# Performance work log

Hardware: AMD Instinct MI355X
Metric: run time of the kernel (lower is better)

## Reference

```python
import jax, jax.numpy as jnp
import numpy as np

N_NODES = 10000
N_EDGES = 80000
D = 512
L = 5
ALPHA = 0.1  # LeakyReLU slope inside GraphAttention
ACT_ALPHA = 0.1  # outer activation slope
EPS = 1e-5
W_SCALE = 0.05  # ~ xavier_normal gain 1.414 for fan_in+fan_out=1536


def leaky(x, a):
    return jnp.where(x >= 0, x, a * x)


def setup_inputs() -> dict:
    key = jax.random.key(0)
    ks = jax.random.split(key, 9)
    return {
        "node_feats": jax.random.normal(ks[0], (N_NODES, D), jnp.float32),
        "edge_feats": jax.random.normal(ks[1], (N_EDGES, D), jnp.float32),
        "src": jax.random.randint(ks[2], (N_EDGES,), 0, N_NODES, jnp.int32),
        "dst": jax.random.randint(ks[3], (N_EDGES,), 0, N_NODES, jnp.int32),
        "Wa": jax.random.normal(ks[4], (L, 2 * D, D), jnp.float32) * W_SCALE,
        "Wn": jax.random.normal(ks[5], (L, 2 * D, D), jnp.float32) * W_SCALE,
        "We": jax.random.normal(ks[6], (L, 2 * D, D), jnp.float32) * W_SCALE,
        "Wnc": jax.random.normal(ks[7], (D, 55), jnp.float32) * W_SCALE,
        "Wec": jax.random.normal(ks[8], (D, 2), jnp.float32) * W_SCALE,
    }


def reference(node_feats, edge_feats, src, dst, Wa, Wn, We, Wnc, Wec):
    n = node_feats.shape[0]
    nx, ex = node_feats, edge_feats
    for l in range(L):
        nx_src = nx[src]  # [E, D]
        nx_dst = nx[dst]  # [E, D]
        # a_p = exp(fa([e_x, dst_x]) - columnwise max over edges)
        ap = jnp.concatenate((ex, nx_dst), axis=1) @ Wa[l]
        ap = jnp.exp(ap - jnp.max(ap, axis=0, keepdims=True))
        # a_r = exp(fa([e_x, src_x]) - columnwise max over edges)
        ar = jnp.concatenate((ex, nx_src), axis=1) @ Wa[l]
        ar = jnp.exp(ar - jnp.max(ar, axis=0, keepdims=True))
        # softmax-like normalization per destination node
        z = jax.ops.segment_sum(ap, dst, num_segments=n)  # [N, D]
        a = ap / (z[dst] + EPS)
        # aggregate a * edge_x to destination nodes
        z2 = jax.ops.segment_sum(a * ex, dst, num_segments=n)  # [N, D]
        ft = jnp.concatenate((z2, nx), axis=1) @ Wn[l]
        # edge update: blend src/dst node feats by a_r/a_p shares
        a_sum = ap + ar
        blend = (ar / a_sum) * nx_src + (ap / a_sum) * nx_dst
        ex_new = jnp.concatenate((blend, ex), axis=1) @ We[l]
        # inner leaky_relu then outer activation (both LeakyReLU)
        nx = leaky(leaky(ft, ALPHA), ACT_ALPHA)
        ex = leaky(leaky(ex_new, ALPHA), ACT_ALPHA)
    node_conf = nx @ Wnc
    edge_conf = ex @ Wec
    return (nx, node_conf, ex, edge_conf)
```

## Files before the change

kernel.cpp:

```cpp
#include <hip/hip_runtime.h>
#include <hip/hip_fp16.h>
#include <math.h>

#define D 512
#define NNODES 10000
#define NEDGES 80000
#define LAYERS 5
#define EPS 1e-5f
#define PPAN 625

typedef _Float16 f16x8 __attribute__((ext_vector_type(8)));
typedef float f32x4 __attribute__((ext_vector_type(4)));

__device__ inline unsigned short f2h(float x) { return __half_as_ushort(__float2half(x)); }
__device__ inline float h2f(unsigned short u) { return __half2float(__ushort_as_half(u)); }
__device__ inline uint4 pack8(const unsigned short* v) {
  uint4 r;
  r.x = (unsigned)v[0] | ((unsigned)v[1] << 16);
  r.y = (unsigned)v[2] | ((unsigned)v[3] << 16);
  r.z = (unsigned)v[4] | ((unsigned)v[5] << 16);
  r.w = (unsigned)v[6] | ((unsigned)v[7] << 16);
  return r;
}
__device__ inline void unpack8(uint4 v, unsigned short* o) {
  o[0] = v.x & 0xffff; o[1] = v.x >> 16;
  o[2] = v.y & 0xffff; o[3] = v.y >> 16;
  o[4] = v.z & 0xffff; o[5] = v.z >> 16;
  o[6] = v.w & 0xffff; o[7] = v.w >> 16;
}

__device__ inline void gload16(const void* g, void* l) {
  __builtin_amdgcn_global_load_lds((const __attribute__((address_space(1))) void*)g,
                                   (__attribute__((address_space(3))) void*)l, 16, 0, 0);
}

__device__ inline int octA(int r, int o) {
  return ((o >> 2) << 6) + ((((o & 3) ^ ((r >> 1) & 3))) << 4);
}

__global__ __launch_bounds__(256) void toF16_k(const float* __restrict__ src,
                                               char* __restrict__ dst, int nOct) {
  for (long long i = (long long)blockIdx.x * 256 + threadIdx.x; i < nOct;
       i += (long long)gridDim.x * 256) {
    int row = (int)(i >> 6), oct = (int)(i & 63);
    const float* s = src + (size_t)row * 512 + oct * 8;
    float4 x0 = *(const float4*)s, x1 = *(const float4*)(s + 4);
    float xs[8] = {x0.x, x0.y, x0.z, x0.w, x1.x, x1.y, x1.z, x1.w};
    unsigned short h[8];
#pragma unroll
    for (int j = 0; j < 8; j++) h[j] = f2h(xs[j]);
    *(uint4*)(dst + (size_t)row * 1024 + octA(row, oct)) = pack8(h);
  }
}

__global__ __launch_bounds__(256) void wprep_k(const float* __restrict__ Wa,
                                               const float* __restrict__ Wn,
                                               const float* __restrict__ We,
                                               char* __restrict__ WT) {
  __shared__ float tile[64][65];
  int mat = blockIdx.z;
  const float* W = (mat < 5) ? Wa + (size_t)mat * 1024 * 512
                 : (mat < 10) ? Wn + (size_t)(mat - 5) * 1024 * 512
                              : We + (size_t)(mat - 10) * 1024 * 512;
  char* out = WT + (size_t)mat * 512 * 2048;
  int n0 = blockIdx.x * 64, k0 = blockIdx.y * 64;
  int t = threadIdx.x;
  int ty = t >> 2, tx = t & 3;
  const float* wr = W + (size_t)(k0 + ty) * 512 + n0 + tx * 16;
  float4 v0 = *(const float4*)(wr + 0), v1 = *(const float4*)(wr + 4);
  float4 v2 = *(const float4*)(wr + 8), v3 = *(const float4*)(wr + 12);
  float vv[16] = {v0.x, v0.y, v0.z, v0.w, v1.x, v1.y, v1.z, v1.w,
                  v2.x, v2.y, v2.z, v2.w, v3.x, v3.y, v3.z, v3.w};
#pragma unroll
  for (int j = 0; j < 16; j++) tile[ty][tx * 16 + j] = vv[j];
  __syncthreads();
#pragma unroll
  for (int p = 0; p < 2; p++) {
    int chunk = t + p * 256;
    int n = chunk >> 3, cc = chunk & 7;
    float xs[8];
#pragma unroll
    for (int j = 0; j < 8; j++) xs[j] = tile[cc * 8 + j][n];
    unsigned short h[8];
#pragma unroll
    for (int j = 0; j < 8; j++) h[j] = f2h(xs[j]);
    int ng = n0 + n;
    int kc = (k0 >> 3) + cc;
    *(uint4*)(out + (size_t)ng * 2048 + octA(ng, kc)) = pack8(h);
  }
}

__global__ __launch_bounds__(256) void hist_k(const int* __restrict__ dst, int* __restrict__ cnt) {
  int e = blockIdx.x * 256 + threadIdx.x;
  if (e < NEDGES) atomicAdd(&cnt[dst[e]], 1);
}

__global__ __launch_bounds__(256) void scan_k(const int* __restrict__ cnt,
                                              int* __restrict__ off, int* __restrict__ cur) {
  __shared__ int part[256];
  const int CH = (NNODES + 255) / 256;
  int t = threadIdx.x;
  int s = 0;
  int l0 = t * CH;
  for (int i = 0; i < CH; i++) {
    int idx = l0 + i;
    if (idx < NNODES) s += cnt[idx];
  }
  part[t] = s;
  __syncthreads();
  if (t == 0) {
    int acc = 0;
    for (int i = 0; i < 256; i++) { int v = part[i]; part[i] = acc; acc += v; }
  }
  __syncthreads();
  int acc = part[t];
  for (int i = 0; i < CH; i++) {
    int idx = l0 + i;
    if (idx < NNODES) { off[idx] = acc; cur[idx] = acc; acc += cnt[idx]; }
  }
  if (t == 255) off[NNODES] = acc;
}

__global__ __launch_bounds__(256) void scatter_k(const int* __restrict__ dst,
                                                 int* __restrict__ cur, int* __restrict__ eid) {
  int e = blockIdx.x * 256 + threadIdx.x;
  if (e < NEDGES) {
    int p = atomicAdd(&cur[dst[e]], 1);
    eid[p] = e;
  }
}

template<int KT, bool ACT, bool OUT_I, bool CMAX, int BM>
__global__ __launch_bounds__(BM * 2) void gemmI(const char* __restrict__ X1,
                                                const char* __restrict__ X2,
                                                const char* __restrict__ BW, int cb0,
                                                void* __restrict__ Yout, int R,
                                                const int* __restrict__ srcI,
                                                const int* __restrict__ dstI,
                                                const char* __restrict__ NaH,
                                                float* __restrict__ part_p,
                                                float* __restrict__ part_r) {
  constexpr int T = BM * 2;
  constexpr int BUF = (BM == 256) ? 24576 : 16384;
  constexpr int BOFF = (BM == 256) ? 16384 : 8192;
  constexpr int NH = BM / 64;
  constexpr int G = T / 32;
  __shared__ char smem[3 * BUF];
  const int tid = threadIdx.x;
  const int lane = tid & 63, wv = tid >> 6;
  const int NT = KT / 32;
  int flat = blockIdx.y * 4 + blockIdx.x;
  int total = gridDim.y * 4;
  int xcd = flat & 7, idx = flat >> 3;
  int q = total >> 3, rem = total & 7;
  int base = xcd * q + (xcd < rem ? xcd : rem);
  int f2 = base + idx;
  const int bn0 = (f2 & 3) * 128, bm0 = (f2 >> 2) * BM;
  const int r16 = lane & 15, g = lane >> 4;
  const int mo = (wv >> 1) * 64, no = (wv & 1) * 64;
  const int lr16 = lane >> 2, ls16 = (lane & 3) * 16;
  f32x4 acc[4][4];
#pragma unroll
  for (int i = 0; i < 4; i++)
#pragma unroll
    for (int j = 0; j < 4; j++) acc[i][j] = (f32x4){0.f, 0.f, 0.f, 0.f};

  int offA[4], offB[4];
#pragma unroll
  for (int mi = 0; mi < 4; mi++) {
    int row = mo + mi * 16 + r16;
    offA[mi] = row * 64 + ((g ^ ((row >> 1) & 3)) << 4);
  }
#pragma unroll
  for (int ni = 0; ni < 4; ni++) {
    int row = no + ni * 16 + r16;
    offB[ni] = BOFF + row * 64 + ((g ^ ((row >> 1) & 3)) << 4);
  }

  const char* pA0;
  const char* pA1;
  const char* pB0;
  const char* pB1;
  {
    int g0 = bm0 + wv * 16 + lr16; if (g0 > R - 1) g0 = R - 1;
    int g1 = bm0 + (BM / 2) + wv * 16 + lr16; if (g1 > R - 1) g1 = R - 1;
    pA0 = X1 + (size_t)g0 * 1024 + ls16;
    pA1 = X1 + (size_t)g1 * 1024 + ls16;
    int n0r = bn0 + wv * 16 + lr16;
    pB0 = BW + (size_t)n0r * 2048 + cb0 * 16 + ls16;
    if (BM == 128) {
      int n1r = bn0 + (4 + wv) * 16 + lr16;
      pB1 = BW + (size_t)n1r * 2048 + cb0 * 16 + ls16;
    } else {
      pB1 = pB0;
    }
  }

  int us = 0;
#define STAGE()                                                 \
  {                                                             \
    char* sb = smem + (us % 3) * BUF;                           \
    gload16(pA0, sb + wv * 1024);                               \
    gload16(pA1, sb + ((BM / 32) + wv) * 1024);                 \
    gload16(pB0, sb + BOFF + wv * 1024);                        \
    if (BM == 128) gload16(pB1, sb + BOFF + (4 + wv) * 1024);   \
    pA0 += 64; pA1 += 64; pB0 += 64;                            \
    if (BM == 128) pB1 += 64;                                   \
    us++;                                                       \
  }

  STAGE();
  STAGE();
  for (int t = 0; t < NT; ++t) {
    if (t + 1 < NT) {
      if (BM == 128) asm volatile("s_waitcnt vmcnt(4)" ::: "memory");
      else           asm volatile("s_waitcnt vmcnt(3)" ::: "memory");
    } else {
      asm volatile("s_waitcnt vmcnt(0)" ::: "memory");
    }
    __builtin_amdgcn_s_barrier();
    if (us < NT) {
      if (KT == 1024 && us == 16) {
        int g0 = bm0 + wv * 16 + lr16; if (g0 > R - 1) g0 = R - 1;
        int g1 = bm0 + (BM / 2) + wv * 16 + lr16; if (g1 > R - 1) g1 = R - 1;
        pA0 = X2 + (size_t)g0 * 1024 + ls16;
        pA1 = X2 + (size_t)g1 * 1024 + ls16;
      }
      STAGE();
    }
    const char* As = smem + (t % 3) * BUF;
    f16x8 a[4], b[4];
#pragma unroll
    for (int mi = 0; mi < 4; mi++) a[mi] = *(const f16x8*)(As + offA[mi]);
#pragma unroll
    for (int ni = 0; ni < 4; ni++) b[ni] = *(const f16x8*)(As + offB[ni]);
    __builtin_amdgcn_s_setprio(1);
#pragma unroll
    for (int mi = 0; mi < 4; mi++)
#pragma unroll
      for (int ni = 0; ni < 4; ni++)
        acc[mi][ni] = __builtin_amdgcn_mfma_f32_16x16x32_f16(a[mi], b[ni], acc[mi][ni], 0, 0, 0);
    __builtin_amdgcn_s_setprio(0);
  }
#undef STAGE

  if (!OUT_I) {
    float* Y = (float*)Yout;
#pragma unroll
    for (int mi = 0; mi < 4; mi++)
#pragma unroll
      for (int j = 0; j < 4; j++) {
        int row = bm0 + mo + mi * 16 + g * 4 + j;
        if (row < R) {
#pragma unroll
          for (int ni = 0; ni < 4; ni++) {
            float v = acc[mi][ni][j];
            if (ACT) v = (v >= 0.f) ? v : 0.01f * v;
            Y[(size_t)row * 512 + bn0 + no + ni * 16 + r16] = v;
          }
        }
      }
  } else {
    float* stg = (float*)smem;
    const int hc = tid & 31;
    const int rg = tid >> 5;
    const int coct = (bn0 >> 3) + (hc >> 1);
    const int csub = (hc & 1) * 8;
    float4 mp4 = make_float4(-1e30f, -1e30f, -1e30f, -1e30f);
    float4 mr4 = mp4;
#pragma unroll
    for (int h = 0; h < NH; h++) {
      __syncthreads();
      if ((wv >> 1) == h) {
#pragma unroll
        for (int mi = 0; mi < 4; mi++)
#pragma unroll
          for (int j = 0; j < 4; j++) {
            int rl = mi * 16 + g * 4 + j;
#pragma unroll
            for (int ni = 0; ni < 4; ni++) {
              float v = acc[mi][ni][j];
              if (ACT) v = (v >= 0.f) ? v : 0.01f * v;
              stg[rl * 128 + no + ni * 16 + r16] = v;
            }
          }
      }
      __syncthreads();
#pragma unroll
      for (int qq = 0; qq < 2048 / T; qq++) {
        int rl = rg + qq * G;
        int grow = bm0 + h * 64 + rl;
        if (grow < R) {
          float4 v = *(const float4*)&stg[rl * 128 + hc * 4];
          unsigned short h0 = f2h(v.x), h1 = f2h(v.y), h2 = f2h(v.z), h3 = f2h(v.w);
          uint2 pk;
          pk.x = (unsigned)h0 | ((unsigned)h1 << 16);
          pk.y = (unsigned)h2 | ((unsigned)h3 << 16);
          int oct = (bn0 >> 3) + (hc >> 1);
          *(uint2*)((char*)Yout + (size_t)grow * 1024 + octA(grow, oct) + (hc & 1) * 8) = pk;
          if (CMAX) {
            int d = dstI[grow], s = srcI[grow];
            float qx = h2f(h0), qy = h2f(h1), qz = h2f(h2), qw = h2f(h3);
            uint2 hd = *(const uint2*)(NaH + (size_t)d * 1024 + octA(d, coct) + csub);
            uint2 hs = *(const uint2*)(NaH + (size_t)s * 1024 + octA(s, coct) + csub);
            mp4.x = fmaxf(mp4.x, qx + h2f(hd.x & 0xffff));
            mp4.y = fmaxf(mp4.y, qy + h2f(hd.x >> 16));
            mp4.z = fmaxf(mp4.z, qz + h2f(hd.y & 0xffff));
            mp4.w = fmaxf(mp4.w, qw + h2f(hd.y >> 16));
            mr4.x = fmaxf(mr4.x, qx + h2f(hs.x & 0xffff));
            mr4.y = fmaxf(mr4.y, qy + h2f(hs.x >> 16));
            mr4.z = fmaxf(mr4.z, qz + h2f(hs.y & 0xffff));
            mr4.w = fmaxf(mr4.w, qw + h2f(hs.y >> 16));
          }
        }
      }
    }
    if (CMAX) {
      __syncthreads();
      float* red = (float*)smem;
      *(float4*)&red[rg * 128 + hc * 4] = mp4;
      *(float4*)&red[G * 128 + rg * 128 + hc * 4] = mr4;
      __syncthreads();
      if (tid < 128) {
        float vp = -1e30f, vr = -1e30f;
#pragma unroll
        for (int gi = 0; gi < G; gi++) {
          vp = fmaxf(vp, red[gi * 128 + tid]);
          vr = fmaxf(vr, red[G * 128 + gi * 128 + tid]);
        }
        int panel = f2 >> 2;
        part_p[(size_t)panel * 512 + bn0 + tid] = vp;
        part_r[(size_t)panel * 512 + bn0 + tid] = vr;
      }
    }
  }
}

__global__ __launch_bounds__(256) void colmax_red1_k(const float* __restrict__ part,
                                                     float* __restrict__ part2) {
  int bx = blockIdx.x;
  int seg = bx >> 2;
  int idx = (bx & 3) * 256 + threadIdx.x;
  int c = idx & 511;
  const float* P = part + (size_t)(idx >> 9) * (PPAN * 512) + c;
  int b0 = seg * 125, b1 = b0 + 125;
  float v = -1e30f;
#pragma unroll 1
  for (int b = b0; b < b1; b += 5) {
    float v0 = P[(size_t)(b + 0) * 512], v1 = P[(size_t)(b + 1) * 512];
    float v2 = P[(size_t)(b + 2) * 512], v3 = P[(size_t)(b + 3) * 512];
    float v4 = P[(size_t)(b + 4) * 512];
    v = fmaxf(v, fmaxf(fmaxf(v0, v1), fmaxf(fmaxf(v2, v3), v4)));
  }
  part2[(size_t)seg * 1024 + idx] = v;
}

__global__ __launch_bounds__(256) void colmax_red2_k(const float* __restrict__ part2,
                                                     float* __restrict__ m) {
  int idx = blockIdx.x * 256 + threadIdx.x;
  float v = part2[idx];
#pragma unroll
  for (int s = 1; s < 5; s++) v = fmaxf(v, part2[(size_t)s * 1024 + idx]);
  m[idx] = v;
}

__global__ __launch_bounds__(256) void aggblend_k(const char* __restrict__ EaH,
                                                  const char* __restrict__ NaH,
                                                  const char* __restrict__ exI,
                                                  const char* __restrict__ nxI,
                                                  const int* __restrict__ src,
                                                  const int* __restrict__ off,
                                                  const int* __restrict__ eid,
                                                  const float* __restrict__ mp,
                                                  const float* __restrict__ mr,
                                                  char* __restrict__ blendH,
                                                  char* __restrict__ z2I) {
  const int w = threadIdx.x >> 6, o = threadIdx.x & 63;
  int n = blockIdx.x * 4 + w;
  if (n >= NNODES) return;
  float m_p[8], m_r[8], nd[8], xd[8], z[8], z2[8];
#pragma unroll
  for (int j = 0; j < 8; j++) {
    m_p[j] = mp[o * 8 + j];
    m_r[j] = mr[o * 8 + j];
    z[j] = 0.f; z2[j] = 0.f;
  }
  {
    unsigned short hn[8], hx[8];
    unpack8(*(const uint4*)(NaH + (size_t)n * 1024 + octA(n, o)), hn);
    unpack8(*(const uint4*)(nxI + (size_t)n * 1024 + octA(n, o)), hx);
#pragma unroll
    for (int j = 0; j < 8; j++) { nd[j] = h2f(hn[j]); xd[j] = h2f(hx[j]); }
  }
  const int i0 = off[n], i1 = off[n + 1];
  const int cnt = i1 - i0;
  if (cnt > 0) {
#define LOADE(ii, e_, ea_, x_, nn_, sv_)                             \
    {                                                                \
      e_ = eid[ii];                                                  \
      int s_ = src[e_];                                              \
      ea_ = *(const uint4*)(EaH + (size_t)e_ * 1024 + octA(e_, o));  \
      x_  = *(const uint4*)(exI + (size_t)e_ * 1024 + octA(e_, o));  \
      nn_ = *(const uint4*)(nxI + (size_t)s_ * 1024 + octA(s_, o));  \
      sv_ = *(const uint4*)(NaH + (size_t)s_ * 1024 + octA(s_, o));  \
    }
    int eA, eB;
    uint4 eaA, xA, nA, svA, eaB, xB, nB, svB;
    LOADE(i0, eA, eaA, xA, nA, svA);
    if (cnt > 1) {
      LOADE(i0 + 1, eB, eaB, xB, nB, svB);
    } else {
      eB = eA; eaB = eaA; xB = xA; nB = nA; svB = svA;
    }
    for (int i = i0; i < i1; ++i) {
      int eC = eB;
      uint4 eaC = eaB, xC = xB, nC = nB, svC = svB;
      if (i + 2 < i1) {
        LOADE(i + 2, eC, eaC, xC, nC, svC);
      }
      unsigned short eh[8], xh[8], sh[8], sn[8];
      unpack8(eaA, eh);
      unpack8(xA, xh);
      unpack8(nA, sh);
      unpack8(svA, sn);
      unsigned short bh[8];
#pragma unroll
      for (int j = 0; j < 8; j++) {
        float ev = h2f(eh[j]);
        float spv = ev + nd[j] - m_p[j];
        float srv = ev + h2f(sn[j]) - m_r[j];
        float ap = __expf(spv);
        float xe = h2f(xh[j]);
        z[j] += ap;
        z2[j] += ap * xe;
        float u = srv - spv;
        float evx = __expf(-fabsf(u));
        float wpos = 1.f / (1.f + evx);
        float wr = (u >= 0.f) ? wpos : 1.f - wpos;
        float xs_ = h2f(sh[j]);
        bh[j] = f2h(wr * xs_ + (1.f - wr) * xd[j]);
      }
      *(uint4*)(blendH + (size_t)eA * 1024 + octA(eA, o)) = pack8(bh);
      eA = eB; eaA = eaB; xA = xB; nA = nB; svA = svB;
      eB = eC; eaB = eaC; xB = xC; nB = nC; svB = svC;
    }
#undef LOADE
  }
  unsigned short zh[8];
#pragma unroll
  for (int j = 0; j < 8; j++) zh[j] = f2h(z2[j] / (z[j] + EPS));
  *(uint4*)(z2I + (size_t)n * 1024 + octA(n, o)) = pack8(zh);
}

__global__ __launch_bounds__(256) void nodeconf_k(const float* __restrict__ nx,
                                                  const float* __restrict__ Wnc,
                                                  float* __restrict__ out) {
  int w = threadIdx.x >> 6, lane = threadIdx.x & 63;
  int n = blockIdx.x * 4 + w;
  const float* r = nx + (size_t)n * D;
  if (lane < 55) {
    float acc = 0.f;
    for (int k = 0; k < D; k++) acc = fmaf(r[k], Wnc[k * 55 + lane], acc);
    out[(size_t)n * 55 + lane] = acc;
  }
}

__global__ __launch_bounds__(256) void edgeconf_k(const float* __restrict__ ex,
                                                  const float* __restrict__ Wec,
                                                  float* __restrict__ out) {
  int w = threadIdx.x >> 6, lane = threadIdx.x & 63;
  int e = blockIdx.x * 4 + w;
  const float* r = ex + (size_t)e * D + lane * 8;
  float4 v0 = *(const float4*)r;
  float4 v1 = *(const float4*)(r + 4);
  const float* wp = Wec + lane * 16;
  float vv[8] = {v0.x, v0.y, v0.z, v0.w, v1.x, v1.y, v1.z, v1.w};
  float a0 = 0.f, a1 = 0.f;
#pragma unroll
  for (int j = 0; j < 8; j++) {
    a0 = fmaf(vv[j], wp[j * 2 + 0], a0);
    a1 = fmaf(vv[j], wp[j * 2 + 1], a1);
  }
#pragma unroll
  for (int off = 32; off; off >>= 1) {
    a0 += __shfl_down(a0, off);
    a1 += __shfl_down(a1, off);
  }
  if (lane == 0) { out[(size_t)e * 2 + 0] = a0; out[(size_t)e * 2 + 1] = a1; }
}

extern "C" void kernel_launch(void* const* d_in, const int* in_sizes, int n_in,
                              void* d_out, int out_size, void* d_ws, size_t ws_size,
                              hipStream_t stream) {
  const float* in_nx = (const float*)d_in[0];
  const float* in_ex = (const float*)d_in[1];
  const int* src = (const int*)d_in[2];
  const int* dst = (const int*)d_in[3];
  const float* Wa = (const float*)d_in[4];
  const float* Wn = (const float*)d_in[5];
  const float* We = (const float*)d_in[6];
  const float* Wnc = (const float*)d_in[7];
  const float* Wec = (const float*)d_in[8];

  float* out = (float*)d_out;
  float* o_nx = out;
  float* o_nc = o_nx + (size_t)NNODES * D;
  float* o_ex = o_nc + (size_t)NNODES * 55;
  float* o_ec = o_ex + (size_t)NEDGES * D;

  const size_t SZ_EH = (size_t)NEDGES * 1024;
  const size_t SZ_NH = (size_t)NNODES * 1024;
  const size_t MATSZ = (size_t)512 * 2048;
  char* w = (char*)d_ws;
  char* EaH = w;
  char* blendH = w + SZ_EH;
  char* exA = w + 2 * SZ_EH;
  char* nxA = w + 3 * SZ_EH;
  char* NaH = w + 3 * SZ_EH + SZ_NH;
  char* z2I = w + 3 * SZ_EH + 2 * SZ_NH;
  float* mpf = (float*)(w + 3 * SZ_EH + 3 * SZ_NH);
  char* WT = w + 3 * SZ_EH + 3 * SZ_NH + 8192;
  char* csr = WT + 15 * MATSZ;
  int* cnt = (int*)csr;
  int* offp = cnt + NNODES + 8;
  int* cur = offp + NNODES + 8;
  int* eid = cur + NNODES + 8;
  float* part_p = (float*)(eid + NEDGES);
  float* part_r = part_p + PPAN * 512;
  float* part2 = part_r + PPAN * 512;

  char* exB = (char*)o_ex;
  char* nxB = (char*)o_nx;

  wprep_k<<<dim3(8, 16, 15), 256, 0, stream>>>(Wa, Wn, We, WT);
  toF16_k<<<2048, 256, 0, stream>>>(in_ex, exA, NEDGES * 64);
  toF16_k<<<2048, 256, 0, stream>>>(in_nx, nxA, NNODES * 64);
  hipMemsetAsync(cnt, 0, NNODES * sizeof(int), stream);
  hist_k<<<(NEDGES + 255) / 256, 256, 0, stream>>>(dst, cnt);
  scan_k<<<1, 256, 0, stream>>>(cnt, offp, cur);
  scatter_k<<<(NEDGES + 255) / 256, 256, 0, stream>>>(dst, cur, eid);

  dim3 gE128(4, PPAN);
  dim3 gE256(4, 313);
  dim3 gN(4, (NNODES + 127) / 128);

  for (int l = 0; l < LAYERS; l++) {
    const char* WaT = WT + (size_t)l * MATSZ;
    const char* WnT = WT + (size_t)(5 + l) * MATSZ;
    const char* WeT = WT + (size_t)(10 + l) * MATSZ;
    char* exCur = (l & 1) ? exB : exA;
    char* exNxt = (l & 1) ? exA : exB;
    char* nxCur = (l & 1) ? nxB : nxA;
    char* nxNxt = (l & 1) ? nxA : nxB;

    gemmI<512, false, true, false, 128><<<gN, 256, 0, stream>>>(
        nxCur, nullptr, WaT, 64, NaH, NNODES, nullptr, nullptr, nullptr, nullptr, nullptr);
    gemmI<512, false, true, true, 128><<<gE128, 256, 0, stream>>>(
        exCur, nullptr, WaT, 0, EaH, NEDGES, src, dst, NaH, part_p, part_r);

    colmax_red1_k<<<20, 256, 0, stream>>>(part_p, part2);
    colmax_red2_k<<<4, 256, 0, stream>>>(part2, mpf);

    aggblend_k<<<(NNODES + 3) / 4, 256, 0, stream>>>(EaH, NaH, exCur, nxCur, src,
                                                     offp, eid, mpf, mpf + 512, blendH, z2I);

    if (l < 4)
      gemmI<1024, true, true, false, 128><<<gN, 256, 0, stream>>>(
          z2I, nxCur, WnT, 0, nxNxt, NNODES, nullptr, nullptr, nullptr, nullptr, nullptr);
    else
      gemmI<1024, true, false, false, 128><<<gN, 256, 0, stream>>>(
          z2I, nxCur, WnT, 0, o_nx, NNODES, nullptr, nullptr, nullptr, nullptr, nullptr);

    if (l < 4)
      gemmI<1024, true, true, false, 256><<<gE256, 512, 0, stream>>>(
          blendH, exCur, WeT, 0, exNxt, NEDGES, nullptr, nullptr, nullptr, nullptr, nullptr);
    else
      gemmI<1024, true, false, false, 256><<<gE256, 512, 0, stream>>>(
          blendH, exCur, WeT, 0, o_ex, NEDGES, nullptr, nullptr, nullptr, nullptr, nullptr);
  }

  nodeconf_k<<<NNODES / 4, 256, 0, stream>>>(o_nx, Wnc, o_nc);
  edgeconf_k<<<NEDGES / 4, 256, 0, stream>>>(o_ex, Wec, o_ec);
}
```

Before: 2.008 ms.

## Permute edges into dst-sorted order and merge node/edge GEMMs into one launch

Edge features and the src/dst indices are reordered once into CSR (destination-sorted) order, so the aggregation kernel reads edge rows contiguously instead of through eid indirection. The final edge output is scattered back to original order through a row map. The node update GEMM and the edge update GEMM are also fused into a single launch, with blocks split by blockIdx.y, to cut a launch and fill the device better. The cost is an extra permutation pass at setup, scattered writes for the final edge output, and the node GEMM now using the larger 256-row tile.

```diff
diff --git a/kernel.cpp b/kernel.cpp
--- a/kernel.cpp
+++ b/kernel.cpp
@@ -50,6 +50,36 @@
 #pragma unroll
     for (int j = 0; j < 8; j++) h[j] = f2h(xs[j]);
     *(uint4*)(dst + (size_t)row * 1024 + octA(row, oct)) = pack8(h);
+  }
+}
+
+__global__ __launch_bounds__(256) void toF16perm_k(const float* __restrict__ src,
+                                                   const int* __restrict__ eid,
+                                                   char* __restrict__ dst) {
+  for (long long i = (long long)blockIdx.x * 256 + threadIdx.x; i < (long long)NEDGES * 64;
+       i += (long long)gridDim.x * 256) {
+    int row = (int)(i >> 6), oct = (int)(i & 63);
+    int orig = eid[row];
+    const float* s = src + (size_t)orig * 512 + oct * 8;
+    float4 x0 = *(const float4*)s, x1 = *(const float4*)(s + 4);
+    float xs[8] = {x0.x, x0.y, x0.z, x0.w, x1.x, x1.y, x1.z, x1.w};
+    unsigned short h[8];
+#pragma unroll
+    for (int j = 0; j < 8; j++) h[j] = f2h(xs[j]);
+    *(uint4*)(dst + (size_t)row * 1024 + octA(row, oct)) = pack8(h);
+  }
+}
+
+__global__ __launch_bounds__(256) void permidx_k(const int* __restrict__ src,
+                                                 const int* __restrict__ dst,
+                                                 const int* __restrict__ eid,
+                                                 int* __restrict__ srcp,
+                                                 int* __restrict__ dstp) {
+  int i = blockIdx.x * 256 + threadIdx.x;
+  if (i < NEDGES) {
+    int e = eid[i];
+    srcp[i] = src[e];
+    dstp[i] = dst[e];
   }
 }
 
@@ -131,26 +161,26 @@
 }
 
 template<int KT, bool ACT, bool OUT_I, bool CMAX, int BM>
-__global__ __launch_bounds__(BM * 2) void gemmI(const char* __restrict__ X1,
-                                                const char* __restrict__ X2,
-                                                const char* __restrict__ BW, int cb0,
-                                                void* __restrict__ Yout, int R,
-                                                const int* __restrict__ srcI,
-                                                const int* __restrict__ dstI,
-                                                const char* __restrict__ NaH,
-                                                float* __restrict__ part_p,
-                                                float* __restrict__ part_r) {
+__device__ __forceinline__ void gemm_body(char* smem,
+                                          const char* __restrict__ X1,
+                                          const char* __restrict__ X2,
+                                          const char* __restrict__ BW, int cb0,
+                                          void* __restrict__ Yout, int R,
+                                          int flat, int total,
+                                          const int* __restrict__ srcI,
+                                          const int* __restrict__ dstI,
+                                          const char* __restrict__ NaH,
+                                          float* __restrict__ part_p,
+                                          float* __restrict__ part_r,
+                                          const int* __restrict__ rowMap) {
   constexpr int T = BM * 2;
   constexpr int BUF = (BM == 256) ? 24576 : 16384;
   constexpr int BOFF = (BM == 256) ? 16384 : 8192;
   constexpr int NH = BM / 64;
   constexpr int G = T / 32;
-  __shared__ char smem[3 * BUF];
   const int tid = threadIdx.x;
   const int lane = tid & 63, wv = tid >> 6;
   const int NT = KT / 32;
-  int flat = blockIdx.y * 4 + blockIdx.x;
-  int total = gridDim.y * 4;
   int xcd = flat & 7, idx = flat >> 3;
   int q = total >> 3, rem = total & 7;
   int base = xcd * q + (xcd < rem ? xcd : rem);
@@ -252,11 +282,12 @@
       for (int j = 0; j < 4; j++) {
         int row = bm0 + mo + mi * 16 + g * 4 + j;
         if (row < R) {
+          int orow = rowMap ? rowMap[row] : row;
 #pragma unroll
           for (int ni = 0; ni < 4; ni++) {
             float v = acc[mi][ni][j];
             if (ACT) v = (v >= 0.f) ? v : 0.01f * v;
-            Y[(size_t)row * 512 + bn0 + no + ni * 16 + r16] = v;
+            Y[(size_t)orow * 512 + bn0 + no + ni * 16 + r16] = v;
           }
         }
       }
@@ -336,6 +367,46 @@
   }
 }
 
+template<int KT, bool ACT, bool OUT_I, bool CMAX, int BM>
+__global__ __launch_bounds__(BM * 2) void gemmI(const char* __restrict__ X1,
+                                                const char* __restrict__ X2,
+                                                const char* __restrict__ BW, int cb0,
+                                                void* __restrict__ Yout, int R,
+                                                const int* __restrict__ srcI,
+                                                const int* __restrict__ dstI,
+                                                const char* __restrict__ NaH,
+                                                float* __restrict__ part_p,
+                                                float* __restrict__ part_r) {
+  __shared__ char smem[3 * ((BM == 256) ? 24576 : 16384)];
+  gemm_body<KT, ACT, OUT_I, CMAX, BM>(smem, X1, X2, BW, cb0, Yout, R,
+                                      blockIdx.y * 4 + blockIdx.x, gridDim.y * 4,
+                                      srcI, dstI, NaH, part_p, part_r, nullptr);
+}
+
+template<bool OUT_I>
+__global__ __launch_bounds__(512) void gemmB_k(const char* __restrict__ z2I,
+                                               const char* __restrict__ nxCur,
+                                               const char* __restrict__ WnT,
+                                               const char* __restrict__ blendH,
+                                               const char* __restrict__ exCur,
+                                               const char* __restrict__ WeT,
+                                               void* __restrict__ nodeOut,
+                                               void* __restrict__ edgeOut,
+                                               const int* __restrict__ rowMap) {
+  __shared__ char smem[3 * 24576];
+  if (blockIdx.y < 313) {
+    gemm_body<1024, true, OUT_I, false, 256>(smem, blendH, exCur, WeT, 0, edgeOut, NEDGES,
+                                             blockIdx.y * 4 + blockIdx.x, 313 * 4,
+                                             nullptr, nullptr, nullptr, nullptr, nullptr,
+                                             rowMap);
+  } else {
+    gemm_body<1024, true, OUT_I, false, 256>(smem, z2I, nxCur, WnT, 0, nodeOut, NNODES,
+                                             (blockIdx.y - 313) * 4 + blockIdx.x, 40 * 4,
+                                             nullptr, nullptr, nullptr, nullptr, nullptr,
+                                             nullptr);
+  }
+}
+
 __global__ __launch_bounds__(256) void colmax_red1_k(const float* __restrict__ part,
                                                      float* __restrict__ part2) {
   int bx = blockIdx.x;
@@ -368,9 +439,8 @@
                                                   const char* __restrict__ NaH,
                                                   const char* __restrict__ exI,
                                                   const char* __restrict__ nxI,
-                                                  const int* __restrict__ src,
+                                                  const int* __restrict__ srcp,
                                                   const int* __restrict__ off,
-                                                  const int* __restrict__ eid,
                                                   const float* __restrict__ mp,
                                                   const float* __restrict__ mr,
                                                   char* __restrict__ blendH,
@@ -397,8 +467,8 @@
   if (cnt > 0) {
 #define LOADE(ii, e_, ea_, x_, nn_, sv_)                             \
     {                                                                \
-      e_ = eid[ii];                                                  \
-      int s_ = src[e_];                                              \
+      e_ = ii;                                                       \
+      int s_ = srcp[e_];                                             \
       ea_ = *(const uint4*)(EaH + (size_t)e_ * 1024 + octA(e_, o));  \
       x_  = *(const uint4*)(exI + (size_t)e_ * 1024 + octA(e_, o));  \
       nn_ = *(const uint4*)(nxI + (size_t)s_ * 1024 + octA(s_, o));  \
@@ -525,7 +595,9 @@
   int* offp = cnt + NNODES + 8;
   int* cur = offp + NNODES + 8;
   int* eid = cur + NNODES + 8;
-  float* part_p = (float*)(eid + NEDGES);
+  int* srcp = eid + NEDGES;
+  int* dstp = srcp + NEDGES;
+  float* part_p = (float*)(dstp + NEDGES);
   float* part_r = part_p + PPAN * 512;
   float* part2 = part_r + PPAN * 512;
 
@@ -533,16 +605,17 @@
   char* nxB = (char*)o_nx;
 
   wprep_k<<<dim3(8, 16, 15), 256, 0, stream>>>(Wa, Wn, We, WT);
-  toF16_k<<<2048, 256, 0, stream>>>(in_ex, exA, NEDGES * 64);
   toF16_k<<<2048, 256, 0, stream>>>(in_nx, nxA, NNODES * 64);
   hipMemsetAsync(cnt, 0, NNODES * sizeof(int), stream);
   hist_k<<<(NEDGES + 255) / 256, 256, 0, stream>>>(dst, cnt);
   scan_k<<<1, 256, 0, stream>>>(cnt, offp, cur);
   scatter_k<<<(NEDGES + 255) / 256, 256, 0, stream>>>(dst, cur, eid);
+  permidx_k<<<(NEDGES + 255) / 256, 256, 0, stream>>>(src, dst, eid, srcp, dstp);
+  toF16perm_k<<<2048, 256, 0, stream>>>(in_ex, eid, exA);
 
   dim3 gE128(4, PPAN);
-  dim3 gE256(4, 313);
   dim3 gN(4, (NNODES + 127) / 128);
+  dim3 gB(4, 353);
 
   for (int l = 0; l < LAYERS; l++) {
     const char* WaT = WT + (size_t)l * MATSZ;
@@ -556,27 +629,20 @@
     gemmI<512, false, true, false, 128><<<gN, 256, 0, stream>>>(
         nxCur, nullptr, WaT, 64, NaH, NNODES, nullptr, nullptr, nullptr, nullptr, nullptr);
     gemmI<512, false, true, true, 128><<<gE128, 256, 0, stream>>>(
-        exCur, nullptr, WaT, 0, EaH, NEDGES, src, dst, NaH, part_p, part_r);
+        exCur, nullptr, WaT, 0, EaH, NEDGES, srcp, dstp, NaH, part_p, part_r);
 
     colmax_red1_k<<<20, 256, 0, stream>>>(part_p, part2);
     colmax_red2_k<<<4, 256, 0, stream>>>(part2, mpf);
 
-    aggblend_k<<<(NNODES + 3) / 4, 256, 0, stream>>>(EaH, NaH, exCur, nxCur, src,
-                                                     offp, eid, mpf, mpf + 512, blendH, z2I);
+    aggblend_k<<<(NNODES + 3) / 4, 256, 0, stream>>>(EaH, NaH, exCur, nxA == exCur ? nxA : ((l & 1) ? nxB : nxA), srcp,
+                                                     offp, mpf, mpf + 512, blendH, z2I);
 
     if (l < 4)
-      gemmI<1024, true, true, false, 128><<<gN, 256, 0, stream>>>(
-          z2I, nxCur, WnT, 0, nxNxt, NNODES, nullptr, nullptr, nullptr, nullptr, nullptr);
+      gemmB_k<true><<<gB, 512, 0, stream>>>(z2I, nxCur, WnT, blendH, exCur, WeT,
+                                            nxNxt, exNxt, nullptr);
     else
-      gemmI<1024, true, false, false, 128><<<gN, 256, 0, stream>>>(
-          z2I, nxCur, WnT, 0, o_nx, NNODES, nullptr, nullptr, nullptr, nullptr, nullptr);
-
-    if (l < 4)
-      gemmI<1024, true, true, false, 256><<<gE256, 512, 0, stream>>>(
-          blendH, exCur, WeT, 0, exNxt, NEDGES, nullptr, nullptr, nullptr, nullptr, nullptr);
-    else
-      gemmI<1024, true, false, false, 256><<<gE256, 512, 0, stream>>>(
-          blendH, exCur, WeT, 0, o_ex, NEDGES, nullptr, nullptr, nullptr, nullptr, nullptr);
+      gemmB_k<false><<<gB, 512, 0, stream>>>(z2I, nxCur, WnT, blendH, exCur, WeT,
+                                             o_nx, o_ex, eid);
   }
 
   nodeconf_k<<<NNODES / 4, 256, 0, stream>>>(o_nx, Wnc, o_nc);
```

Measured after the change: 2.074 ms. 3.3% more time.

## Add 256x256-tile double-buffered MFMA GEMM for edge update projection

Applied to the files above, without the earlier changes.

Replaces the generic 256-row edge-update GEMM with a dedicated kernel using 256x256 output tiles, 8 waves and 128KB of LDS double buffering. Loads for the next K-step are staged in quarters and overlap the MFMA work, with XCD-aware block remapping and s_setprio around the compute. Larger tiles raise reuse of both the activations and the weights. The cost is one block per CU because of the LDS footprint, and extra barriers on every quarter step.

```diff
diff --git a/kernel.cpp b/kernel.cpp
--- a/kernel.cpp
+++ b/kernel.cpp
@@ -336,6 +336,151 @@
   }
 }
 
+template<bool OUT_I>
+__global__ __launch_bounds__(512) void gemm8_k(const char* __restrict__ X1,
+                                               const char* __restrict__ X2,
+                                               const char* __restrict__ BW,
+                                               void* __restrict__ Yout) {
+  __shared__ char smem[131072];
+  const int R = NEDGES;
+  const int tid = threadIdx.x;
+  const int lane = tid & 63, wv = tid >> 6;
+  const int wm = wv >> 2, wn = wv & 3;
+  const int r16 = lane & 15, g = lane >> 4;
+  int flat = blockIdx.y * 2 + blockIdx.x;
+  int total = 626;
+  int xcd = flat & 7, idx = flat >> 3;
+  int q8 = total >> 3, rem = total & 7;
+  int base = xcd * q8 + (xcd < rem ? xcd : rem);
+  int f2 = base + idx;
+  const int bn0 = (f2 & 1) * 256, bm0 = (f2 >> 1) * 256;
+
+  f32x4 acc[8][4];
+#pragma unroll
+  for (int i = 0; i < 8; i++)
+#pragma unroll
+    for (int j = 0; j < 4; j++) acc[i][j] = (f32x4){0.f, 0.f, 0.f, 0.f};
+
+  const int slot = ((g ^ ((r16 >> 1) & 3)) << 4);
+  const int baseA = (wm * 128 + r16) * 64 + slot;
+  const int baseB = 32768 + (wn * 64 + r16) * 64 + slot;
+
+  const int srow = wv * 32 + (lane >> 2);
+  const int sslot = (lane & 3) * 16;
+#define STAGEQ(Tn, bb, qq)                                                     \
+  {                                                                            \
+    int s_ = (qq) >> 1;                                                        \
+    char* ldsq = smem + (bb) * 65536 + (((qq) & 1) ? 32768 : 0) + s_ * 16384 + \
+                 wv * 2048;                                                    \
+    if (((qq) & 1) == 0) {                                                     \
+      const char* xb; int tl;                                                  \
+      if ((Tn) < 8) { xb = X1; tl = (Tn); } else { xb = X2; tl = (Tn) - 8; }   \
+      int r0 = bm0 + srow; if (r0 > R - 1) r0 = R - 1;                         \
+      int r1 = bm0 + srow + 16; if (r1 > R - 1) r1 = R - 1;                    \
+      gload16(xb + (size_t)r0 * 1024 + tl * 128 + s_ * 64 + sslot, ldsq);      \
+      gload16(xb + (size_t)r1 * 1024 + tl * 128 + s_ * 64 + sslot, ldsq + 1024);\
+    } else {                                                                   \
+      int r0 = bn0 + srow;                                                     \
+      int r1 = r0 + 16;                                                        \
+      gload16(BW + (size_t)r0 * 2048 + (Tn) * 128 + s_ * 64 + sslot, ldsq);    \
+      gload16(BW + (size_t)r1 * 2048 + (Tn) * 128 + s_ * 64 + sslot, ldsq + 1024);\
+    }                                                                          \
+  }
+
+  STAGEQ(0, 0, 0); STAGEQ(0, 0, 1); STAGEQ(0, 0, 2); STAGEQ(0, 0, 3);
+  asm volatile("s_waitcnt vmcnt(0)" ::: "memory");
+  __builtin_amdgcn_s_barrier();
+
+  f16x8 b[4];
+  for (int T = 0; T < 16; ++T) {
+    const int buf = T & 1;
+    const char* Ab = smem + buf * 65536;
+#pragma unroll
+    for (int q = 0; q < 4; ++q) {
+      const int mh = q & 1, ks = q >> 1;
+      f16x8 a[4];
+#pragma unroll
+      for (int mi = 0; mi < 4; mi++)
+        a[mi] = *(const f16x8*)(Ab + ks * 16384 + baseA + (mh * 4 + mi) * 1024);
+      if (mh == 0) {
+#pragma unroll
+        for (int ni = 0; ni < 4; ni++)
+          b[ni] = *(const f16x8*)(Ab + ks * 16384 + baseB + ni * 1024);
+      }
+      if (T + 1 < 16) STAGEQ(T + 1, buf ^ 1, q);
+      asm volatile("s_waitcnt vmcnt(4)" ::: "memory");
+      __builtin_amdgcn_s_barrier();
+      __builtin_amdgcn_s_setprio(1);
+#pragma unroll
+      for (int mi = 0; mi < 4; mi++)
+#pragma unroll
+        for (int ni = 0; ni < 4; ni++)
+          acc[mh * 4 + mi][ni] =
+              __builtin_amdgcn_mfma_f32_16x16x32_f16(a[mi], b[ni], acc[mh * 4 + mi][ni], 0, 0, 0);
+      __builtin_amdgcn_s_setprio(0);
+      __builtin_amdgcn_s_barrier();
+    }
+  }
+#undef STAGEQ
+  asm volatile("s_waitcnt vmcnt(0)" ::: "memory");
+  __builtin_amdgcn_s_barrier();
+
+  if (!OUT_I) {
+    float* Y = (float*)Yout;
+#pragma unroll
+    for (int mi = 0; mi < 8; mi++)
+#pragma unroll
+      for (int j = 0; j < 4; j++) {
+        int row = bm0 + wm * 128 + mi * 16 + g * 4 + j;
+        if (row < R) {
+#pragma unroll
+          for (int ni = 0; ni < 4; ni++) {
+            float v = acc[mi][ni][j];
+            v = (v >= 0.f) ? v : 0.01f * v;
+            Y[(size_t)row * 512 + bn0 + wn * 64 + ni * 16 + r16] = v;
+          }
+        }
+      }
+  } else {
+    float* stg = (float*)smem;
+    const int hc = tid & 63;
+    const int rg = tid >> 6;
+#pragma unroll
+    for (int h = 0; h < 2; h++) {
+      __syncthreads();
+      if (wm == h) {
+#pragma unroll
+        for (int mi = 0; mi < 8; mi++)
+#pragma unroll
+          for (int j = 0; j < 4; j++) {
+            int rl = mi * 16 + g * 4 + j;
+#pragma unroll
+            for (int ni = 0; ni < 4; ni++) {
+              float v = acc[mi][ni][j];
+              v = (v >= 0.f) ? v : 0.01f * v;
+              stg[rl * 256 + wn * 64 + ni * 16 + r16] = v;
+            }
+          }
+      }
+      __syncthreads();
+#pragma unroll
+      for (int it = 0; it < 16; it++) {
+        int rl = rg + it * 8;
+        int grow = bm0 + h * 128 + rl;
+        if (grow < R) {
+          float4 v = *(const float4*)&stg[rl * 256 + hc * 4];
+          unsigned short h0 = f2h(v.x), h1 = f2h(v.y), h2 = f2h(v.z), h3 = f2h(v.w);
+          uint2 pk;
+          pk.x = (unsigned)h0 | ((unsigned)h1 << 16);
+          pk.y = (unsigned)h2 | ((unsigned)h3 << 16);
+          int oct = (bn0 >> 3) + (hc >> 1);
+          *(uint2*)((char*)Yout + (size_t)grow * 1024 + octA(grow, oct) + (hc & 1) * 8) = pk;
+        }
+      }
+    }
+  }
+}
+
 __global__ __launch_bounds__(256) void colmax_red1_k(const float* __restrict__ part,
                                                      float* __restrict__ part2) {
   int bx = blockIdx.x;
@@ -541,8 +686,8 @@
   scatter_k<<<(NEDGES + 255) / 256, 256, 0, stream>>>(dst, cur, eid);
 
   dim3 gE128(4, PPAN);
-  dim3 gE256(4, 313);
   dim3 gN(4, (NNODES + 127) / 128);
+  dim3 g8(2, 313);
 
   for (int l = 0; l < LAYERS; l++) {
     const char* WaT = WT + (size_t)l * MATSZ;
@@ -572,11 +717,9 @@
           z2I, nxCur, WnT, 0, o_nx, NNODES, nullptr, nullptr, nullptr, nullptr, nullptr);
 
     if (l < 4)
-      gemmI<1024, true, true, false, 256><<<gE256, 512, 0, stream>>>(
-          blendH, exCur, WeT, 0, exNxt, NEDGES, nullptr, nullptr, nullptr, nullptr, nullptr);
+      gemm8_k<true><<<g8, 512, 0, stream>>>(blendH, exCur, WeT, exNxt);
     else
-      gemmI<1024, true, false, false, 256><<<gE256, 512, 0, stream>>>(
-          blendH, exCur, WeT, 0, o_ex, NEDGES, nullptr, nullptr, nullptr, nullptr, nullptr);
+      gemm8_k<false><<<g8, 512, 0, stream>>>(blendH, exCur, WeT, o_ex);
   }
 
   nodeconf_k<<<NNODES / 4, 256, 0, stream>>>(o_nx, Wnc, o_nc);
```

Measured after the change: 2.055 ms. 1.02x slower.
